# Kernel optimization log

Measured on AMD Instinct MI355X. Metric: run time of the kernel, lower is better.

The kernel has to match this reference:

```python
import jax, jax.numpy as jnp
import numpy as np


def setup_inputs() -> dict:
    key = jax.random.key(0)
    ks = jax.random.split(key, 7)
    B, C, W, H = 4, 256, 64, 64
    C8 = C // 8
    return {
        "x": jax.random.normal(ks[0], (B, C, W, H), dtype=jnp.float32),
        "Wq": jax.random.normal(ks[1], (C8, C), dtype=jnp.float32) * 0.05,
        "bq": jax.random.normal(ks[2], (C8,), dtype=jnp.float32) * 0.05,
        "Wk": jax.random.normal(ks[3], (C8, C), dtype=jnp.float32) * 0.05,
        "bk": jax.random.normal(ks[4], (C8,), dtype=jnp.float32) * 0.05,
        "Wv": jax.random.normal(ks[5], (C, C), dtype=jnp.float32) * 0.05,
        "bv": jax.random.normal(ks[6], (C,), dtype=jnp.float32) * 0.05,
    }


def reference(x, Wq, bq, Wk, bk, Wv, bv):
    B, C, W, H = x.shape
    N = W * H
    xf = x.reshape(B, C, N)  # flatten spatial dims
    # 1x1 convs == per-position linear projections
    q = jnp.einsum('oc,bcn->bno', Wq, xf) + bq            # (B, N, C/8)
    k = jnp.einsum('oc,bcn->bon', Wk, xf) + bk[None, :, None]  # (B, C/8, N)
    # attention scores (B, N, N); original applies softmax over dim=1
    attn = jax.nn.softmax(jnp.einsum('bno,bom->bnm', q, k), axis=1)
    v = jnp.einsum('oc,bcn->bno', Wv, xf) + bv            # (B, N, C)
    out = jnp.einsum('bnm,bmc->bnc', attn, v)             # (B, N, C)
    # faithful to original: raw view of (B, N, C) as (B, C, W, H)
    return out.reshape(B, C, W, H)
```

## Files before the change

### kernel.cpp

```cpp
#include <hip/hip_runtime.h>
#include <math.h>

#define NB 4
#define CC 256
#define CO 32
#define NN 4096
#define MU 320
#define LOG2E 1.44269504088896f

typedef __attribute__((ext_vector_type(4))) float f4;
typedef __attribute__((ext_vector_type(8))) short s8;
typedef __attribute__((ext_vector_type(8))) unsigned short us8;
typedef __attribute__((ext_vector_type(2))) unsigned int u2;
typedef __attribute__((ext_vector_type(4))) unsigned int u4i;

__device__ __forceinline__ unsigned short f2bf(float f) {
    unsigned int u = __float_as_uint(f);
    u = (u + 0x7FFFu + ((u >> 16) & 1u)) >> 16;
    return (unsigned short)u;
}
__device__ __forceinline__ unsigned int cvtpk(float lo, float hi) {
    unsigned int r;
    asm("v_cvt_pk_bf16_f32 %0, %1, %2" : "=v"(r) : "v"(lo), "v"(hi));
    return r;
}
__device__ __forceinline__ int swz128(int row, int colByte) {
    return row * 128 + (colByte ^ ((row & 7) << 4));
}
#define LDS_BARRIER() asm volatile("s_waitcnt lgkmcnt(0)\n\ts_barrier" ::: "memory")

union s8u4 { s8 s; u4i u; };

__global__ __launch_bounds__(256) void prepw_kernel(
    const float* __restrict__ Wq, const float* __restrict__ bq,
    const float* __restrict__ Wk, const float* __restrict__ bk,
    const float* __restrict__ Wv, const float* __restrict__ bv,
    unsigned short* __restrict__ Wb, float* __restrict__ fb)
{
    const int t = threadIdx.x;
    #pragma unroll
    for (int i = 0; i < 4; ++i) {
        const int e = blockIdx.x * 1024 + i * 256 + t;
        const int u = e >> 8, c = e & 255;
        float val = (u < 32) ? Wq[u * 256 + c]
                  : (u < 64) ? Wk[(u - 32) * 256 + c]
                             : Wv[(u - 64) * 256 + c];
        Wb[e] = f2bf(val);
    }
    if (blockIdx.x == 0) {
        for (int u = t; u < MU; u += 256)
            fb[u] = (u < 32) ? bq[u] : (u < 64) ? bk[u - 32] : bv[u - 64];
    }
}

__global__ __launch_bounds__(256) void projf_kernel(
    const float* __restrict__ x, const unsigned short* __restrict__ Wb,
    const float* __restrict__ fb,
    unsigned short* __restrict__ qb, unsigned short* __restrict__ kb,
    unsigned short* __restrict__ vtb)
{
    __shared__ float xl[16][260];

    const int t   = threadIdx.x;
    const int b   = blockIdx.x >> 8;
    const int nbl = blockIdx.x & 255;
    const int n0  = nbl * 16;

    {
        const int nl = t & 3;
        const int c8 = t >> 2;
        #pragma unroll
        for (int pass = 0; pass < 4; ++pass) {
            const int c = c8 + pass * 64;
            f4 xv = *reinterpret_cast<const f4*>(x + ((size_t)(b * CC + c)) * NN + n0 + nl * 4);
            #pragma unroll
            for (int j = 0; j < 4; ++j) xl[nl * 4 + j][c] = xv[j];
        }
    }
    __syncthreads();

    const int w   = t >> 6;
    const int l   = t & 63;
    const int l15 = l & 15;
    const int g4  = l >> 4;
    const int n   = n0 + l15;

    s8 bfr[8];
    #pragma unroll
    for (int kk = 0; kk < 8; ++kk) {
        f4 a  = *reinterpret_cast<const f4*>(&xl[l15][kk * 32 + g4 * 8]);
        f4 c2 = *reinterpret_cast<const f4*>(&xl[l15][kk * 32 + g4 * 8 + 4]);
        s8u4 tmp;
        tmp.u = (u4i){ cvtpk(a[0], a[1]), cvtpk(a[2], a[3]),
                       cvtpk(c2[0], c2[1]), cvtpk(c2[2], c2[3]) };
        bfr[kk] = tmp.s;
    }

    const f4 z = {0.f, 0.f, 0.f, 0.f};
    unsigned short* qrow = qb + ((size_t)(b * NN + n)) * CO;
    unsigned short* krow = kb + ((size_t)(b * NN + n)) * CO;

    #pragma unroll
    for (int i = 0; i < 5; ++i) {
        const int u0 = (w * 5 + i) * 16;
        f4 acc = z;
        #pragma unroll
        for (int kk = 0; kk < 8; ++kk) {
            s8 af = *reinterpret_cast<const s8*>(Wb + (size_t)(u0 + l15) * CC + kk * 32 + g4 * 8);
            acc = __builtin_amdgcn_mfma_f32_16x16x32_bf16(af, bfr[kk], acc, 0, 0, 0);
        }
        f4 bias4 = *reinterpret_cast<const f4*>(fb + u0 + g4 * 4);
        if (u0 < 32) {
            u2 pw = { cvtpk((acc[0] + bias4[0]) * LOG2E, (acc[1] + bias4[1]) * LOG2E),
                      cvtpk((acc[2] + bias4[2]) * LOG2E, (acc[3] + bias4[3]) * LOG2E) };
            *reinterpret_cast<u2*>(qrow + u0 + g4 * 4) = pw;
        } else if (u0 < 64) {
            u2 pw = { cvtpk(acc[0] + bias4[0], acc[1] + bias4[1]),
                      cvtpk(acc[2] + bias4[2], acc[3] + bias4[3]) };
            *reinterpret_cast<u2*>(krow + (u0 - 32) + g4 * 4) = pw;
        } else {
            const int cbase = u0 - 64 + g4 * 4;
            #pragma unroll
            for (int r = 0; r < 4; ++r)
                vtb[((size_t)(b * CC + cbase + r)) * NN + n] = f2bf(acc[r] + bias4[r]);
        }
    }
}

__global__ __launch_bounds__(256) void colstats_kernel(
    const unsigned short* __restrict__ qb, const unsigned short* __restrict__ kb,
    const unsigned short* __restrict__ vtb, unsigned short* __restrict__ vfr)
{
    __shared__ float red[4][16];
    __shared__ float civl[16];

    const int t   = threadIdx.x;
    const int b   = blockIdx.x >> 8;
    const int mb  = blockIdx.x & 255;
    const int l   = t & 63;
    const int w   = t >> 6;
    const int l15 = l & 15;
    const int g4  = l >> 4;
    const int m   = mb * 16 + l15;

    const unsigned short* qbB = qb + (size_t)b * NN * CO;
    s8 kfrag = *reinterpret_cast<const s8*>(kb + ((size_t)b * NN + m) * CO + g4 * 8);

    const f4 z = {0.f, 0.f, 0.f, 0.f};
    float ssum = 0.f;

    const int nbeg = w * 1024, nend = nbeg + 1024;
    for (int n0 = nbeg; n0 < nend; n0 += 32) {
        s8 a0 = *reinterpret_cast<const s8*>(qbB + (size_t)(n0 + l15) * CO + g4 * 8);
        s8 a1 = *reinterpret_cast<const s8*>(qbB + (size_t)(n0 + 16 + l15) * CO + g4 * 8);
        f4 d0 = __builtin_amdgcn_mfma_f32_16x16x32_bf16(a0, kfrag, z, 0, 0, 0);
        f4 d1 = __builtin_amdgcn_mfma_f32_16x16x32_bf16(a1, kfrag, z, 0, 0, 0);
        #pragma unroll
        for (int r = 0; r < 4; ++r) ssum += exp2f(d0[r]) + exp2f(d1[r]);
    }

    ssum += __shfl_xor(ssum, 16);
    ssum += __shfl_xor(ssum, 32);
    if (l < 16) red[w][l15] = ssum;
    __syncthreads();
    if (w == 0 && l < 16)
        civl[l15] = 1.0f / (red[0][l15] + red[1][l15] + red[2][l15] + red[3][l15]);
    __syncthreads();

    const int mt   = mb >> 2;
    const int ksl  = (mb >> 1) & 1;
    const int g4b  = (mb & 1) * 2;
    const int cg   = t >> 4;
    const int l15v = t & 15;
    const unsigned short* vp = vtb + ((size_t)(b * CC + t)) * NN + mb * 16;
    unsigned short* dst = vfr + (size_t)b * 1048576
                        + (((mt * 16 + cg) * 2 + ksl) << 9)
                        + (g4b * 16 + l15v) * 8;
    #pragma unroll
    for (int i = 0; i < 2; ++i) {
        us8 vv = *reinterpret_cast<const us8*>(vp + i * 8);
        u4i o;
        #pragma unroll
        for (int e2 = 0; e2 < 4; ++e2) {
            float f0 = __uint_as_float((unsigned int)vv[2 * e2]     << 16) * civl[i * 8 + 2 * e2];
            float f1 = __uint_as_float((unsigned int)vv[2 * e2 + 1] << 16) * civl[i * 8 + 2 * e2 + 1];
            o[e2] = cvtpk(f0, f1);
        }
        *reinterpret_cast<u4i*>(dst + i * 128) = o;
    }
}

__global__ __launch_bounds__(512, 4) void attn_kernel(
    const unsigned short* __restrict__ qb, const unsigned short* __restrict__ kb,
    const unsigned short* __restrict__ vfr, float* __restrict__ out)
{
    __shared__ __align__(16) char plds[2][32 * 128];

    const int t   = threadIdx.x;
    const int w   = t >> 6;
    const int l   = t & 63;
    const int l15 = l & 15;
    const int g4  = l >> 4;
    const int bid  = (blockIdx.x & 7) * 64 + (blockIdx.x >> 3);
    const int b    = bid >> 7;
    const int nblk = bid & 127;
    const int n0   = nblk * 32;
    const int ng   = w >> 2;
    const int mq   = w & 3;

    const unsigned short* qbB = qb + (size_t)b * NN * CO;
    const unsigned short* kbB = kb + (size_t)b * NN * CO;

    s8 qfrag = *reinterpret_cast<const s8*>(qbB + (size_t)(n0 + ng * 16 + l15) * CO + g4 * 8);

    const int pwo  = swz128(ng * 16 + l15, mq * 32 + g4 * 8);
    const int pr00 = swz128(l15,      g4 * 16);
    const int pr01 = swz128(l15,      64 + g4 * 16);
    const int pr10 = swz128(16 + l15, g4 * 16);
    const int pr11 = swz128(16 + l15, 64 + g4 * 16);

    const unsigned short* kp = kbB + (size_t)(mq * 16 + l15) * CO + g4 * 8;
    const unsigned short* vp = vfr + (size_t)b * 1048576 + w * 2048 + l * 8;

    s8 kreg;
    s8 v0, v1, v2, v3;
    const f4 z = {0.f, 0.f, 0.f, 0.f};
    f4 acc00 = z, acc01 = z, acc10 = z, acc11 = z;

#define LOADK() do { kreg = *reinterpret_cast<const s8*>(kp); kp += 2048; } while (0)
#define LOADV() do { \
        v0 = *reinterpret_cast<const s8*>(vp); \
        v1 = *reinterpret_cast<const s8*>(vp + 512); \
        v2 = *reinterpret_cast<const s8*>(vp + 1024); \
        v3 = *reinterpret_cast<const s8*>(vp + 1536); \
        vp += 16384; \
    } while (0)

#define STAGE(BUF, KR) do { \
        f4 d = __builtin_amdgcn_mfma_f32_16x16x32_bf16(KR, qfrag, z, 0, 0, 0); \
        u2 pw = { cvtpk(exp2f(d[0]), exp2f(d[1])), cvtpk(exp2f(d[2]), exp2f(d[3])) }; \
        *reinterpret_cast<u2*>(plds[BUF] + pwo) = pw; \
    } while (0)

#define PVSTEP(BUF) do { \
        s8 pa00 = *reinterpret_cast<const s8*>(plds[BUF] + pr00); \
        s8 pa01 = *reinterpret_cast<const s8*>(plds[BUF] + pr01); \
        s8 pa10 = *reinterpret_cast<const s8*>(plds[BUF] + pr10); \
        s8 pa11 = *reinterpret_cast<const s8*>(plds[BUF] + pr11); \
        __builtin_amdgcn_s_setprio(1); \
        acc00 = __builtin_amdgcn_mfma_f32_16x16x32_bf16(pa00, v0, acc00, 0, 0, 0); \
        acc01 = __builtin_amdgcn_mfma_f32_16x16x32_bf16(pa00, v2, acc01, 0, 0, 0); \
        acc10 = __builtin_amdgcn_mfma_f32_16x16x32_bf16(pa10, v0, acc10, 0, 0, 0); \
        acc11 = __builtin_amdgcn_mfma_f32_16x16x32_bf16(pa10, v2, acc11, 0, 0, 0); \
        acc00 = __builtin_amdgcn_mfma_f32_16x16x32_bf16(pa01, v1, acc00, 0, 0, 0); \
        acc01 = __builtin_amdgcn_mfma_f32_16x16x32_bf16(pa01, v3, acc01, 0, 0, 0); \
        acc10 = __builtin_amdgcn_mfma_f32_16x16x32_bf16(pa11, v1, acc10, 0, 0, 0); \
        acc11 = __builtin_amdgcn_mfma_f32_16x16x32_bf16(pa11, v3, acc11, 0, 0, 0); \
        __builtin_amdgcn_s_setprio(0); \
    } while (0)

    s8 k0 = *reinterpret_cast<const s8*>(kp); kp += 2048;
    LOADK();
    LOADV();
    STAGE(0, k0);
    LDS_BARRIER();

    for (int i = 0; i < 64; i += 2) {
        STAGE(1, kreg);
        if (i < 62) LOADK();
        PVSTEP(0);
        if (i < 63) LOADV();
        LDS_BARRIER();

        if (i + 1 < 63) STAGE(0, kreg);
        if (i + 1 < 62) LOADK();
        PVSTEP(1);
        if (i + 1 < 63) LOADV();
        LDS_BARRIER();
    }

#undef LOADK
#undef LOADV
#undef STAGE
#undef PVSTEP

    float* ob = out + (size_t)b * NN * CC;
    const int cw = w * 32 + l15;
    #pragma unroll
    for (int r = 0; r < 4; ++r) {
        const size_t row0 = (size_t)(n0 + g4 * 4 + r) * CC;
        const size_t row1 = (size_t)(n0 + 16 + g4 * 4 + r) * CC;
        ob[row0 + cw]      = acc00[r];
        ob[row0 + cw + 16] = acc01[r];
        ob[row1 + cw]      = acc10[r];
        ob[row1 + cw + 16] = acc11[r];
    }
}

extern "C" void kernel_launch(void* const* d_in, const int* in_sizes, int n_in,
                              void* d_out, int out_size, void* d_ws, size_t ws_size,
                              hipStream_t stream)
{
    const float* x  = (const float*)d_in[0];
    const float* Wq = (const float*)d_in[1];
    const float* bq = (const float*)d_in[2];
    const float* Wk = (const float*)d_in[3];
    const float* bk = (const float*)d_in[4];
    const float* Wv = (const float*)d_in[5];
    const float* bv = (const float*)d_in[6];
    float* out = (float*)d_out;

    unsigned short* qb  = (unsigned short*)d_ws;
    unsigned short* kb  = qb  + (size_t)NB * NN * CO;
    unsigned short* vtb = kb  + (size_t)NB * NN * CO;
    unsigned short* vfr = vtb + (size_t)NB * CC * NN;
    unsigned short* Wb  = vfr + (size_t)NB * CC * NN;
    float*          fb  = (float*)(Wb + (size_t)MU * CC);

    prepw_kernel<<<dim3(80), dim3(256), 0, stream>>>(Wq, bq, Wk, bk, Wv, bv, Wb, fb);
    projf_kernel<<<dim3(1024), dim3(256), 0, stream>>>(x, Wb, fb, qb, kb, vtb);
    colstats_kernel<<<dim3(1024), dim3(256), 0, stream>>>(qb, kb, vtb, vfr);
    attn_kernel<<<dim3(512), dim3(512), 0, stream>>>(qb, kb, vfr, out);
}
```

Measured before the change: 112.2 us.

## Double attention row tile to 64 per block to halve V reloads

```diff
diff --git a/kernel.cpp b/kernel.cpp
--- a/kernel.cpp
+++ b/kernel.cpp
@@ -190,42 +190,46 @@
     }
 }
 
-__global__ __launch_bounds__(512, 4) void attn_kernel(
+__global__ __launch_bounds__(512, 2) void attn_kernel(
     const unsigned short* __restrict__ qb, const unsigned short* __restrict__ kb,
     const unsigned short* __restrict__ vfr, float* __restrict__ out)
 {
-    __shared__ __align__(16) char plds[2][32 * 128];
+    __shared__ __align__(16) char plds[2][64 * 128];
 
     const int t   = threadIdx.x;
     const int w   = t >> 6;
     const int l   = t & 63;
     const int l15 = l & 15;
     const int g4  = l >> 4;
-    const int bid  = (blockIdx.x & 7) * 64 + (blockIdx.x >> 3);
-    const int b    = bid >> 7;
-    const int nblk = bid & 127;
-    const int n0   = nblk * 32;
-    const int ng   = w >> 2;
+    const int bid  = (blockIdx.x & 7) * 32 + (blockIdx.x >> 3);
+    const int b    = bid >> 6;
+    const int nblk = bid & 63;
+    const int n0   = nblk * 64;
+    const int nh   = w >> 2;
     const int mq   = w & 3;
+    const int cq   = w & 3;
 
     const unsigned short* qbB = qb + (size_t)b * NN * CO;
     const unsigned short* kbB = kb + (size_t)b * NN * CO;
 
-    s8 qfrag = *reinterpret_cast<const s8*>(qbB + (size_t)(n0 + ng * 16 + l15) * CO + g4 * 8);
-
-    const int pwo  = swz128(ng * 16 + l15, mq * 32 + g4 * 8);
-    const int pr00 = swz128(l15,      g4 * 16);
-    const int pr01 = swz128(l15,      64 + g4 * 16);
-    const int pr10 = swz128(16 + l15, g4 * 16);
-    const int pr11 = swz128(16 + l15, 64 + g4 * 16);
+    s8 qf0 = *reinterpret_cast<const s8*>(qbB + (size_t)(n0 + nh * 32 + l15) * CO + g4 * 8);
+    s8 qf1 = *reinterpret_cast<const s8*>(qbB + (size_t)(n0 + nh * 32 + 16 + l15) * CO + g4 * 8);
+
+    const int pwo0 = swz128(nh * 32 + l15,      mq * 32 + g4 * 8);
+    const int pwo1 = swz128(nh * 32 + 16 + l15, mq * 32 + g4 * 8);
+    const int pr00 = swz128(nh * 32 + l15,      g4 * 16);
+    const int pr01 = swz128(nh * 32 + l15,      64 + g4 * 16);
+    const int pr10 = swz128(nh * 32 + 16 + l15, g4 * 16);
+    const int pr11 = swz128(nh * 32 + 16 + l15, 64 + g4 * 16);
 
     const unsigned short* kp = kbB + (size_t)(mq * 16 + l15) * CO + g4 * 8;
-    const unsigned short* vp = vfr + (size_t)b * 1048576 + w * 2048 + l * 8;
+    const unsigned short* vp = vfr + (size_t)b * 1048576 + cq * 4096 + l * 8;
 
     s8 kreg;
-    s8 v0, v1, v2, v3;
+    s8 v0, v1, v2, v3, v4, v5, v6, v7;
     const f4 z = {0.f, 0.f, 0.f, 0.f};
-    f4 acc00 = z, acc01 = z, acc10 = z, acc11 = z;
+    f4 acc00 = z, acc01 = z, acc02 = z, acc03 = z;
+    f4 acc10 = z, acc11 = z, acc12 = z, acc13 = z;
 
 #define LOADK() do { kreg = *reinterpret_cast<const s8*>(kp); kp += 2048; } while (0)
 #define LOADV() do { \
@@ -233,13 +237,20 @@
         v1 = *reinterpret_cast<const s8*>(vp + 512); \
         v2 = *reinterpret_cast<const s8*>(vp + 1024); \
         v3 = *reinterpret_cast<const s8*>(vp + 1536); \
+        v4 = *reinterpret_cast<const s8*>(vp + 2048); \
+        v5 = *reinterpret_cast<const s8*>(vp + 2560); \
+        v6 = *reinterpret_cast<const s8*>(vp + 3072); \
+        v7 = *reinterpret_cast<const s8*>(vp + 3584); \
         vp += 16384; \
     } while (0)
 
 #define STAGE(BUF, KR) do { \
-        f4 d = __builtin_amdgcn_mfma_f32_16x16x32_bf16(KR, qfrag, z, 0, 0, 0); \
-        u2 pw = { cvtpk(exp2f(d[0]), exp2f(d[1])), cvtpk(exp2f(d[2]), exp2f(d[3])) }; \
-        *reinterpret_cast<u2*>(plds[BUF] + pwo) = pw; \
+        f4 d0 = __builtin_amdgcn_mfma_f32_16x16x32_bf16(KR, qf0, z, 0, 0, 0); \
+        f4 d1 = __builtin_amdgcn_mfma_f32_16x16x32_bf16(KR, qf1, z, 0, 0, 0); \
+        u2 pq0 = { cvtpk(exp2f(d0[0]), exp2f(d0[1])), cvtpk(exp2f(d0[2]), exp2f(d0[3])) }; \
+        u2 pq1 = { cvtpk(exp2f(d1[0]), exp2f(d1[1])), cvtpk(exp2f(d1[2]), exp2f(d1[3])) }; \
+        *reinterpret_cast<u2*>(plds[BUF] + pwo0) = pq0; \
+        *reinterpret_cast<u2*>(plds[BUF] + pwo1) = pq1; \
     } while (0)
 
 #define PVSTEP(BUF) do { \
@@ -250,12 +261,20 @@
         __builtin_amdgcn_s_setprio(1); \
         acc00 = __builtin_amdgcn_mfma_f32_16x16x32_bf16(pa00, v0, acc00, 0, 0, 0); \
         acc01 = __builtin_amdgcn_mfma_f32_16x16x32_bf16(pa00, v2, acc01, 0, 0, 0); \
+        acc02 = __builtin_amdgcn_mfma_f32_16x16x32_bf16(pa00, v4, acc02, 0, 0, 0); \
+        acc03 = __builtin_amdgcn_mfma_f32_16x16x32_bf16(pa00, v6, acc03, 0, 0, 0); \
         acc10 = __builtin_amdgcn_mfma_f32_16x16x32_bf16(pa10, v0, acc10, 0, 0, 0); \
         acc11 = __builtin_amdgcn_mfma_f32_16x16x32_bf16(pa10, v2, acc11, 0, 0, 0); \
+        acc12 = __builtin_amdgcn_mfma_f32_16x16x32_bf16(pa10, v4, acc12, 0, 0, 0); \
+        acc13 = __builtin_amdgcn_mfma_f32_16x16x32_bf16(pa10, v6, acc13, 0, 0, 0); \
         acc00 = __builtin_amdgcn_mfma_f32_16x16x32_bf16(pa01, v1, acc00, 0, 0, 0); \
         acc01 = __builtin_amdgcn_mfma_f32_16x16x32_bf16(pa01, v3, acc01, 0, 0, 0); \
+        acc02 = __builtin_amdgcn_mfma_f32_16x16x32_bf16(pa01, v5, acc02, 0, 0, 0); \
+        acc03 = __builtin_amdgcn_mfma_f32_16x16x32_bf16(pa01, v7, acc03, 0, 0, 0); \
         acc10 = __builtin_amdgcn_mfma_f32_16x16x32_bf16(pa11, v1, acc10, 0, 0, 0); \
         acc11 = __builtin_amdgcn_mfma_f32_16x16x32_bf16(pa11, v3, acc11, 0, 0, 0); \
+        acc12 = __builtin_amdgcn_mfma_f32_16x16x32_bf16(pa11, v5, acc12, 0, 0, 0); \
+        acc13 = __builtin_amdgcn_mfma_f32_16x16x32_bf16(pa11, v7, acc13, 0, 0, 0); \
         __builtin_amdgcn_s_setprio(0); \
     } while (0)
 
@@ -285,15 +304,19 @@
 #undef PVSTEP
 
     float* ob = out + (size_t)b * NN * CC;
-    const int cw = w * 32 + l15;
+    const int cb = cq * 64 + l15;
     #pragma unroll
     for (int r = 0; r < 4; ++r) {
-        const size_t row0 = (size_t)(n0 + g4 * 4 + r) * CC;
-        const size_t row1 = (size_t)(n0 + 16 + g4 * 4 + r) * CC;
-        ob[row0 + cw]      = acc00[r];
-        ob[row0 + cw + 16] = acc01[r];
-        ob[row1 + cw]      = acc10[r];
-        ob[row1 + cw + 16] = acc11[r];
+        const size_t row0 = (size_t)(n0 + nh * 32 + g4 * 4 + r) * CC;
+        const size_t row1 = (size_t)(n0 + nh * 32 + 16 + g4 * 4 + r) * CC;
+        ob[row0 + cb]      = acc00[r];
+        ob[row0 + cb + 16] = acc01[r];
+        ob[row0 + cb + 32] = acc02[r];
+        ob[row0 + cb + 48] = acc03[r];
+        ob[row1 + cb]      = acc10[r];
+        ob[row1 + cb + 16] = acc11[r];
+        ob[row1 + cb + 32] = acc12[r];
+        ob[row1 + cb + 48] = acc13[r];
     }
 }
 
@@ -320,5 +343,5 @@
     prepw_kernel<<<dim3(80), dim3(256), 0, stream>>>(Wq, bq, Wk, bk, Wv, bv, Wb, fb);
     projf_kernel<<<dim3(1024), dim3(256), 0, stream>>>(x, Wb, fb, qb, kb, vtb);
     colstats_kernel<<<dim3(1024), dim3(256), 0, stream>>>(qb, kb, vtb, vfr);
-    attn_kernel<<<dim3(512), dim3(512), 0, stream>>>(qb, kb, vfr, out);
-}
+    attn_kernel<<<dim3(256), dim3(512), 0, stream>>>(qb, kb, vfr, out);
+}
```

Result: slower. 118.3 us (+5.4%).

## Split attention key dimension across two blocks and combine partial outputs

Applied to the files above, without the earlier changes.

```diff
diff --git a/kernel.cpp b/kernel.cpp
--- a/kernel.cpp
+++ b/kernel.cpp
@@ -190,26 +190,15 @@
     }
 }
 
-__global__ __launch_bounds__(512, 4) void attn_kernel(
-    const unsigned short* __restrict__ qb, const unsigned short* __restrict__ kb,
-    const unsigned short* __restrict__ vfr, float* __restrict__ out)
+__device__ __forceinline__ void attn_body(
+    const unsigned short* qbB, const unsigned short* kbB,
+    const unsigned short* vfrB, float* dst,
+    int n0, int ntiles, int w, int l15, int g4)
 {
     __shared__ __align__(16) char plds[2][32 * 128];
 
-    const int t   = threadIdx.x;
-    const int w   = t >> 6;
-    const int l   = t & 63;
-    const int l15 = l & 15;
-    const int g4  = l >> 4;
-    const int bid  = (blockIdx.x & 7) * 64 + (blockIdx.x >> 3);
-    const int b    = bid >> 7;
-    const int nblk = bid & 127;
-    const int n0   = nblk * 32;
-    const int ng   = w >> 2;
-    const int mq   = w & 3;
-
-    const unsigned short* qbB = qb + (size_t)b * NN * CO;
-    const unsigned short* kbB = kb + (size_t)b * NN * CO;
+    const int ng = w >> 2;
+    const int mq = w & 3;
 
     s8 qfrag = *reinterpret_cast<const s8*>(qbB + (size_t)(n0 + ng * 16 + l15) * CO + g4 * 8);
 
@@ -220,7 +209,7 @@
     const int pr11 = swz128(16 + l15, 64 + g4 * 16);
 
     const unsigned short* kp = kbB + (size_t)(mq * 16 + l15) * CO + g4 * 8;
-    const unsigned short* vp = vfr + (size_t)b * 1048576 + w * 2048 + l * 8;
+    const unsigned short* vp = vfrB + w * 2048 + (w < 4 ? (l15 + g4 * 16) : (l15 + g4 * 16)) * 0 + ( (w & 63) * 0 ) + ( ( ( (int)(w*0) ) ) ) + ( ( ( (int) ( ( (w*0) ) ) ) ) ) + ( ( ( (int)0 ) ) ) + ( ( ( (int)0 ) ) ) + ( ( ( (int)0 ) ) ) + ( ( l15 * 0 ) ) + ( ( ( (l15 + (g4 << 4)) ) ) * 8 );
 
     s8 kreg;
     s8 v0, v1, v2, v3;
@@ -235,13 +224,11 @@
         v3 = *reinterpret_cast<const s8*>(vp + 1536); \
         vp += 16384; \
     } while (0)
-
 #define STAGE(BUF, KR) do { \
         f4 d = __builtin_amdgcn_mfma_f32_16x16x32_bf16(KR, qfrag, z, 0, 0, 0); \
         u2 pw = { cvtpk(exp2f(d[0]), exp2f(d[1])), cvtpk(exp2f(d[2]), exp2f(d[3])) }; \
         *reinterpret_cast<u2*>(plds[BUF] + pwo) = pw; \
     } while (0)
-
 #define PVSTEP(BUF) do { \
         s8 pa00 = *reinterpret_cast<const s8*>(plds[BUF] + pr00); \
         s8 pa01 = *reinterpret_cast<const s8*>(plds[BUF] + pr01); \
@@ -265,17 +252,17 @@
     STAGE(0, k0);
     LDS_BARRIER();
 
-    for (int i = 0; i < 64; i += 2) {
+    for (int i = 0; i < ntiles; i += 2) {
         STAGE(1, kreg);
-        if (i < 62) LOADK();
+        if (i < ntiles - 2) LOADK();
         PVSTEP(0);
-        if (i < 63) LOADV();
+        if (i < ntiles - 1) LOADV();
         LDS_BARRIER();
 
-        if (i + 1 < 63) STAGE(0, kreg);
-        if (i + 1 < 62) LOADK();
+        if (i + 1 < ntiles - 1) STAGE(0, kreg);
+        if (i + 1 < ntiles - 2) LOADK();
         PVSTEP(1);
-        if (i + 1 < 63) LOADV();
+        if (i + 1 < ntiles - 1) LOADV();
         LDS_BARRIER();
     }
 
@@ -284,17 +271,61 @@
 #undef STAGE
 #undef PVSTEP
 
-    float* ob = out + (size_t)b * NN * CC;
     const int cw = w * 32 + l15;
     #pragma unroll
     for (int r = 0; r < 4; ++r) {
         const size_t row0 = (size_t)(n0 + g4 * 4 + r) * CC;
         const size_t row1 = (size_t)(n0 + 16 + g4 * 4 + r) * CC;
-        ob[row0 + cw]      = acc00[r];
-        ob[row0 + cw + 16] = acc01[r];
-        ob[row1 + cw]      = acc10[r];
-        ob[row1 + cw + 16] = acc11[r];
-    }
+        dst[row0 + cw]      = acc00[r];
+        dst[row0 + cw + 16] = acc01[r];
+        dst[row1 + cw]      = acc10[r];
+        dst[row1 + cw + 16] = acc11[r];
+    }
+}
+
+__global__ __launch_bounds__(512, 4) void attn_kernel(
+    const unsigned short* __restrict__ qb, const unsigned short* __restrict__ kb,
+    const unsigned short* __restrict__ vfr, float* __restrict__ out)
+{
+    const int t   = threadIdx.x;
+    const int w   = t >> 6;
+    const int l   = t & 63;
+    const int bid = (blockIdx.x & 7) * 64 + (blockIdx.x >> 3);
+    const int b   = bid >> 7;
+    const int n0  = (bid & 127) * 32;
+    attn_body(qb + (size_t)b * NN * CO, kb + (size_t)b * NN * CO,
+              vfr + (size_t)b * 1048576, out + (size_t)b * NN * CC,
+              n0, 64, w, l & 15, l >> 4);
+}
+
+__global__ __launch_bounds__(512, 4) void attn_ms_kernel(
+    const unsigned short* __restrict__ qb, const unsigned short* __restrict__ kb,
+    const unsigned short* __restrict__ vfr, float* __restrict__ out,
+    float* __restrict__ part1)
+{
+    const int t   = threadIdx.x;
+    const int w   = t >> 6;
+    const int l   = t & 63;
+    const int sw  = (blockIdx.x & 7) * 128 + (blockIdx.x >> 3);
+    const int b   = sw >> 8;
+    const int rem = sw & 255;
+    const int n0  = (rem >> 1) * 32;
+    const int mh  = rem & 1;
+    float* dst = (mh == 0) ? (out + (size_t)b * NN * CC) : (part1 + (size_t)b * NN * CC);
+    attn_body(qb + (size_t)b * NN * CO,
+              kb + (size_t)b * NN * CO + (size_t)mh * 2048 * CO,
+              vfr + (size_t)b * 1048576 + (size_t)mh * 524288,
+              dst, n0, 32, w, l & 15, l >> 4);
+}
+
+__global__ __launch_bounds__(256) void combine_kernel(
+    float* __restrict__ out, const float* __restrict__ part1)
+{
+    const size_t i = ((size_t)blockIdx.x * 256 + threadIdx.x) * 4;
+    f4 a = *reinterpret_cast<const f4*>(out + i);
+    f4 p = *reinterpret_cast<const f4*>(part1 + i);
+    a += p;
+    *reinterpret_cast<f4*>(out + i) = a;
 }
 
 extern "C" void kernel_launch(void* const* d_in, const int* in_sizes, int n_in,
@@ -316,9 +347,17 @@
     unsigned short* vfr = vtb + (size_t)NB * CC * NN;
     unsigned short* Wb  = vfr + (size_t)NB * CC * NN;
     float*          fb  = (float*)(Wb + (size_t)MU * CC);
+    float*          p1  = (float*)(fb + 512);
+    const size_t needed = ((char*)(p1 + (size_t)NB * NN * CC)) - (char*)d_ws;
 
     prepw_kernel<<<dim3(80), dim3(256), 0, stream>>>(Wq, bq, Wk, bk, Wv, bv, Wb, fb);
     projf_kernel<<<dim3(1024), dim3(256), 0, stream>>>(x, Wb, fb, qb, kb, vtb);
     colstats_kernel<<<dim3(1024), dim3(256), 0, stream>>>(qb, kb, vtb, vfr);
-    attn_kernel<<<dim3(512), dim3(512), 0, stream>>>(qb, kb, vfr, out);
-}
+
+    if (ws_size >= needed) {
+        attn_ms_kernel<<<dim3(1024), dim3(512), 0, stream>>>(qb, kb, vfr, out, p1);
+        combine_kernel<<<dim3((NB * NN * CC) / 1024), dim3(256), 0, stream>>>(out, p1);
+    } else {
+        attn_kernel<<<dim3(512), dim3(512), 0, stream>>>(qb, kb, vfr, out);
+    }
+}
```

Measured after the change: 122.2 us. 1.09x slower.
